# Performance work log

Measured on AMD Instinct MI355X. Metric: run time of the kernel, lower is better.

Reference implementation:

```python
import jax, jax.numpy as jnp
import numpy as np

N_M = 100000   # metric nodes
N_A = 20000    # alert nodes
E_C = 1600000  # metric->metric 'correlation' edges
E_K = 800000   # metric->alert 'cause' edges
F_IN = 64      # raw feature dim (lazy in_channels in PyG)
DIMS = [128, 256]  # out_dim // 2**(num_layers-i-1) for lstm_dim=256, num_layers=2
NEG_SLOPE = 0.01   # nn.LeakyReLU default


def _lin(key, fan_in, fan_out):
    s = 1.0 / np.sqrt(fan_in)
    return jax.random.uniform(key, (fan_in, fan_out), minval=-s, maxval=s, dtype=jnp.float32)


def setup_inputs() -> dict:
    key = jax.random.key(0)
    ks = jax.random.split(key, 32)
    inp = {
        'x_metric': jax.random.normal(ks[0], (N_M, F_IN), dtype=jnp.float32),
        'x_alert': jax.random.normal(ks[1], (N_A, F_IN), dtype=jnp.float32),
        'w_corr': jax.random.uniform(ks[2], (E_C,), dtype=jnp.float32),
        'w_cause': jax.random.uniform(ks[3], (E_K,), dtype=jnp.float32),
        'src_corr': jax.random.randint(ks[4], (E_C,), 0, N_M, dtype=jnp.int32),
        'dst_corr': jax.random.randint(ks[5], (E_C,), 0, N_M, dtype=jnp.int32),
        'src_cause': jax.random.randint(ks[6], (E_K,), 0, N_M, dtype=jnp.int32),
        'dst_cause': jax.random.randint(ks[7], (E_K,), 0, N_A, dtype=jnp.int32),
    }
    # GraphConv params: lin_rel (with bias) applied to aggregated messages,
    # lin_root (no bias) applied to destination features. Two convs per layer.
    kidx = 8
    in_m, in_a = F_IN, F_IN
    for li, d in enumerate(DIMS):
        inp[f'Wr_c{li}'] = _lin(ks[kidx], in_m, d); kidx += 1  # corr rel
        inp[f'br_c{li}'] = jnp.zeros((d,), jnp.float32)
        inp[f'Wo_c{li}'] = _lin(ks[kidx], in_m, d); kidx += 1  # corr root (dst=metric)
        inp[f'Wr_k{li}'] = _lin(ks[kidx], in_m, d); kidx += 1  # cause rel (src=metric)
        inp[f'br_k{li}'] = jnp.zeros((d,), jnp.float32)
        inp[f'Wo_k{li}'] = _lin(ks[kidx], in_a, d); kidx += 1  # cause root (dst=alert)
        in_m, in_a = d, d
    return inp


def _leaky(x):
    return jnp.where(x > 0, x, NEG_SLOPE * x)


def reference(x_metric, x_alert, w_corr, w_cause,
              src_corr, dst_corr, src_cause, dst_cause,
              Wr_c0, br_c0, Wo_c0, Wr_k0, br_k0, Wo_k0,
              Wr_c1, br_c1, Wo_c1, Wr_k1, br_k1, Wo_k1):
    xm, xa = x_metric, x_alert
    layers = [(Wr_c0, br_c0, Wo_c0, Wr_k0, br_k0, Wo_k0),
              (Wr_c1, br_c1, Wo_c1, Wr_k1, br_k1, Wo_k1)]
    for Wrc, brc, Woc, Wrk, brk, Wok in layers:
        # metric <- metric, GraphConv aggr='add'
        msg_c = xm[src_corr] * w_corr[:, None]                 # [E_C, d_in]
        agg_c = jax.ops.segment_sum(msg_c, dst_corr, num_segments=N_M)
        new_m = agg_c @ Wrc + brc + xm @ Woc
        # alert <- metric, GraphConv aggr='max' (empty segments -> 0, torch_scatter convention)
        msg_k = xm[src_cause] * w_cause[:, None]               # [E_K, d_in]
        agg_k = jax.ops.segment_max(msg_k, dst_cause, num_segments=N_A)
        agg_k = jnp.where(jnp.isfinite(agg_k), agg_k, 0.0)
        new_a = agg_k @ Wrk + brk + xa @ Wok
        xm = _leaky(new_m)
        xa = _leaky(new_a)
    return xa  # HGNN.forward returns x['alert']
```

## Files before the change

### kernel.cpp

```cpp
#include <hip/hip_runtime.h>

#define N_M 100000
#define N_A 20000
#define E_C 1600000
#define E_K 800000
#define CH 2048
#define NXCD 8

typedef __attribute__((ext_vector_type(8)))  short  short8_t;
typedef __attribute__((ext_vector_type(8)))  unsigned short ushort8_t;
typedef __attribute__((ext_vector_type(4)))  unsigned short ushort4_t;
typedef __attribute__((ext_vector_type(4)))  float  f32x4;

__device__ __forceinline__ unsigned short f2b(float f) {
    unsigned u = __float_as_uint(f);
    return (unsigned short)((u + 0x7fffu + ((u >> 16) & 1u)) >> 16);
}
__device__ __forceinline__ float b2f(unsigned short h) {
    return __uint_as_float((unsigned)h << 16);
}

__global__ __launch_bounds__(256) void cast_f32_bf16(const float* __restrict__ in,
                                                     unsigned short* __restrict__ out, int n) {
    int i = (blockIdx.x * 256 + threadIdx.x) * 4;
    if (i >= n) return;
    float4 v = *(const float4*)(in + i);
    ushort4_t o; o.x = f2b(v.x); o.y = f2b(v.y); o.z = f2b(v.z); o.w = f2b(v.w);
    *(ushort4_t*)(out + i) = o;
}

__global__ __launch_bounds__(256) void cast_weights(
    const float* rc0, const float* oc0, const float* rk0, const float* ok0,
    const float* rk1, const float* ok1, unsigned short* __restrict__ wb) {
    int i = (blockIdx.x * 256 + threadIdx.x) * 4;
    if (i >= 98304) return;
    const float* src; int off;
    if      (i < 8192)  { src = rc0; off = 0; }
    else if (i < 16384) { src = oc0; off = 8192; }
    else if (i < 24576) { src = rk0; off = 16384; }
    else if (i < 32768) { src = ok0; off = 24576; }
    else if (i < 65536) { src = rk1; off = 32768; }
    else                { src = ok1; off = 65536; }
    float4 v = *(const float4*)(src + (i - off));
    ushort4_t o; o.x = f2b(v.x); o.y = f2b(v.y); o.z = f2b(v.z); o.w = f2b(v.w);
    *(ushort4_t*)(wb + i) = o;
}


__global__ __launch_bounds__(256) void hist_part(const int* __restrict__ dst,
                                                 int* __restrict__ deg,
                                                 int nE, int nodes_per_part) {
    int chunk = blockIdx.x >> 3, part = blockIdx.x & 7;
    int lo = part * nodes_per_part, hi = lo + nodes_per_part;
    int base = chunk * CH + threadIdx.x;
    #pragma unroll
    for (int k = 0; k < 8; ++k) {
        int e = base + k * 256;
        if (e < nE) {
            int d = __builtin_nontemporal_load(dst + e);
            if (d >= lo && d < hi) atomicAdd(&deg[d], 1);
        }
    }
}

__global__ __launch_bounds__(256) void fill_pay_part(const int* __restrict__ dst,
                                                     const int* __restrict__ src,
                                                     const float* __restrict__ w,
                                                     int* __restrict__ cursor,
                                                     int2* __restrict__ csr_sw,
                                                     int nE, int nodes_per_part) {
    int chunk = blockIdx.x >> 3, part = blockIdx.x & 7;
    int lo = part * nodes_per_part, hi = lo + nodes_per_part;
    int base = chunk * CH + threadIdx.x;
    #pragma unroll
    for (int k = 0; k < 8; ++k) {
        int e = base + k * 256;
        if (e < nE) {
            int d = __builtin_nontemporal_load(dst + e);
            if (d >= lo && d < hi) {
                int p = atomicAdd(&cursor[d], 1);
                int2 sw;
                sw.x = __builtin_nontemporal_load(src + e);
                sw.y = __float_as_int(__builtin_nontemporal_load(w + e));
                csr_sw[p] = sw;
            }
        }
    }
}

__global__ __launch_bounds__(256) void scan_p1(const int* __restrict__ deg,
                                               int* __restrict__ partial, int n) {
    __shared__ int red[256];
    int base = blockIdx.x * CH + threadIdx.x;
    int s = 0;
    #pragma unroll
    for (int k = 0; k < 8; ++k) { int i = base + k * 256; if (i < n) s += deg[i]; }
    red[threadIdx.x] = s; __syncthreads();
    for (int off = 128; off > 0; off >>= 1) {
        if (threadIdx.x < off) red[threadIdx.x] += red[threadIdx.x + off];
        __syncthreads();
    }
    if (threadIdx.x == 0) partial[blockIdx.x] = red[0];
}

__global__ __launch_bounds__(64) void scan_p2(int* __restrict__ partial,
                                              int* __restrict__ rowptr_end, int P) {
    int lane = threadIdx.x;
    int v = (lane < P) ? partial[lane] : 0;
    int incl = v;
    for (int off = 1; off < 64; off <<= 1) {
        int t = __shfl_up(incl, off);
        if (lane >= off) incl += t;
    }
    if (lane < P) partial[lane] = incl - v;
    if (lane == 63) *rowptr_end = incl;
}

__global__ __launch_bounds__(256) void scan_p3(const int* __restrict__ deg,
                                               const int* __restrict__ partial,
                                               int* __restrict__ rowptr,
                                               int* __restrict__ cursor, int n) {
    __shared__ int buf[256];
    int base = blockIdx.x * CH;
    int v[8]; int lsum = 0;
    #pragma unroll
    for (int k = 0; k < 8; ++k) {
        int i = base + threadIdx.x * 8 + k;
        v[k] = (i < n) ? deg[i] : 0; lsum += v[k];
    }
    buf[threadIdx.x] = lsum; __syncthreads();
    for (int off = 1; off < 256; off <<= 1) {
        int t = (threadIdx.x >= off) ? buf[threadIdx.x - off] : 0;
        __syncthreads(); buf[threadIdx.x] += t; __syncthreads();
    }
    int excl = buf[threadIdx.x] - lsum + partial[blockIdx.x];
    #pragma unroll
    for (int k = 0; k < 8; ++k) {
        int i = base + threadIdx.x * 8 + k;
        if (i < n) { rowptr[i] = excl; cursor[i] = excl; }
        excl += v[k];
    }
}

__global__ __launch_bounds__(256) void agg_sum_d64_b(
    const unsigned short* __restrict__ x, const int2* __restrict__ csr_sw,
    const int* __restrict__ rowptr, unsigned short* __restrict__ out, int n) {
    int gw = blockIdx.x * 4 + (threadIdx.x >> 6);
    int lane = threadIdx.x & 63;
    if (gw >= n) return;
    int j = rowptr[gw], end = rowptr[gw + 1];
    float acc = 0.f;
    for (; j + 4 <= end; j += 4) {
        int2 e0 = csr_sw[j], e1 = csr_sw[j+1], e2 = csr_sw[j+2], e3 = csr_sw[j+3];
        float v0 = b2f(x[(size_t)e0.x * 64 + lane]);
        float v1 = b2f(x[(size_t)e1.x * 64 + lane]);
        float v2 = b2f(x[(size_t)e2.x * 64 + lane]);
        float v3 = b2f(x[(size_t)e3.x * 64 + lane]);
        acc = fmaf(v0, __int_as_float(e0.y), acc);
        acc = fmaf(v1, __int_as_float(e1.y), acc);
        acc = fmaf(v2, __int_as_float(e2.y), acc);
        acc = fmaf(v3, __int_as_float(e3.y), acc);
    }
    for (; j < end; ++j) {
        int2 e = csr_sw[j];
        acc = fmaf(b2f(x[(size_t)e.x * 64 + lane]), __int_as_float(e.y), acc);
    }
    out[(size_t)gw * 64 + lane] = f2b(acc);
}

__global__ __launch_bounds__(256) void agg_max_d64_b(
    const unsigned short* __restrict__ x, const int2* __restrict__ csr_sw,
    const int* __restrict__ rowptr, unsigned short* __restrict__ out, int n) {
    int gw = blockIdx.x * 4 + (threadIdx.x >> 6);
    int lane = threadIdx.x & 63;
    if (gw >= n) return;
    int beg = rowptr[gw], end = rowptr[gw + 1];
    float acc = -INFINITY;
    int j = beg;
    for (; j + 4 <= end; j += 4) {
        int2 e0 = csr_sw[j], e1 = csr_sw[j+1], e2 = csr_sw[j+2], e3 = csr_sw[j+3];
        acc = fmaxf(acc, b2f(x[(size_t)e0.x * 64 + lane]) * __int_as_float(e0.y));
        acc = fmaxf(acc, b2f(x[(size_t)e1.x * 64 + lane]) * __int_as_float(e1.y));
        acc = fmaxf(acc, b2f(x[(size_t)e2.x * 64 + lane]) * __int_as_float(e2.y));
        acc = fmaxf(acc, b2f(x[(size_t)e3.x * 64 + lane]) * __int_as_float(e3.y));
    }
    for (; j < end; ++j) {
        int2 e = csr_sw[j];
        acc = fmaxf(acc, b2f(x[(size_t)e.x * 64 + lane]) * __int_as_float(e.y));
    }
    if (beg == end) acc = 0.f;
    out[(size_t)gw * 64 + lane] = f2b(acc);
}

__global__ __launch_bounds__(256) void agg_max_d128_b(
    const unsigned short* __restrict__ x, const int2* __restrict__ csr_sw,
    const int* __restrict__ rowptr, unsigned short* __restrict__ out, int n) {
    int gw = blockIdx.x * 4 + (threadIdx.x >> 6);
    int lane = threadIdx.x & 63;
    if (gw >= n) return;
    int beg = rowptr[gw], end = rowptr[gw + 1];
    float ax = -INFINITY, ay = -INFINITY;
    int j = beg;
    for (; j + 2 <= end; j += 2) {
        int2 e0 = csr_sw[j], e1 = csr_sw[j+1];
        float w0 = __int_as_float(e0.y), w1 = __int_as_float(e1.y);
        unsigned v0 = ((const unsigned*)(x + (size_t)e0.x * 128))[lane];
        unsigned v1 = ((const unsigned*)(x + (size_t)e1.x * 128))[lane];
        ax = fmaxf(ax, b2f((unsigned short)(v0 & 0xffff)) * w0);
        ay = fmaxf(ay, b2f((unsigned short)(v0 >> 16)) * w0);
        ax = fmaxf(ax, b2f((unsigned short)(v1 & 0xffff)) * w1);
        ay = fmaxf(ay, b2f((unsigned short)(v1 >> 16)) * w1);
    }
    for (; j < end; ++j) {
        int2 e = csr_sw[j];
        float ww = __int_as_float(e.y);
        unsigned v = ((const unsigned*)(x + (size_t)e.x * 128))[lane];
        ax = fmaxf(ax, b2f((unsigned short)(v & 0xffff)) * ww);
        ay = fmaxf(ay, b2f((unsigned short)(v >> 16)) * ww);
    }
    if (beg == end) { ax = 0.f; ay = 0.f; }
    ((unsigned*)(out + (size_t)gw * 128))[lane] =
        (unsigned)f2b(ax) | ((unsigned)f2b(ay) << 16);
}

template <int K1, int K2, bool OBF>
__global__ __launch_bounds__(256) void dual_gemm_mfma(
    const unsigned short* __restrict__ A1, const unsigned short* __restrict__ A2,
    const unsigned short* __restrict__ B1, const unsigned short* __restrict__ B2,
    const float* __restrict__ bias, void* __restrict__ out, int M, int N) {
    constexpr int KTOT = K1 + K2;
    constexpr int LB = KTOT + 8;
    __shared__ __align__(16) unsigned short sA[128 * 40];
    __shared__ __align__(16) unsigned short sBT[64 * LB];

    const int tid = threadIdx.x;
    const int lane = tid & 63, wid = tid >> 6;
    const int wm = wid >> 1, wn = wid & 1;
    const int bm0 = blockIdx.y * 128, n0 = blockIdx.x * 64;

    for (int idx = tid; idx < KTOT * 64; idx += 256) {
        int k = idx >> 6, n = idx & 63;
        unsigned short v = (k < K1) ? B1[k * N + n0 + n] : B2[(k - K1) * N + n0 + n];
        sBT[n * LB + k] = v;
    }

    f32x4 acc[4][2];
    #pragma unroll
    for (int i = 0; i < 4; ++i)
        #pragma unroll
        for (int j = 0; j < 2; ++j)
            acc[i][j] = (f32x4){0.f, 0.f, 0.f, 0.f};

    const int kk = (lane >> 4) * 8;
    const int l15 = lane & 15;

    for (int k0 = 0; k0 < KTOT; k0 += 32) {
        __syncthreads();
        #pragma unroll
        for (int i = 0; i < 2; ++i) {
            int v = tid + i * 256;
            int row = v >> 2, kv = (v & 3) * 8;
            int gm = bm0 + row, gk = k0 + kv;
            ushort8_t val = (ushort8_t)0;
            if (gm < M) {
                const unsigned short* src = (gk < K1)
                    ? (A1 + (size_t)gm * K1 + gk)
                    : (A2 + (size_t)gm * K2 + (gk - K1));
                val = *(const ushort8_t*)src;
            }
            *(ushort8_t*)(sA + row * 40 + kv) = val;
        }
        __syncthreads();

        short8_t bfr[2];
        #pragma unroll
        for (int nf = 0; nf < 2; ++nf)
            bfr[nf] = *(const short8_t*)(sBT + (wn * 32 + nf * 16 + l15) * LB + k0 + kk);
        #pragma unroll
        for (int mf = 0; mf < 4; ++mf) {
            short8_t a = *(const short8_t*)(sA + (wm * 64 + mf * 16 + l15) * 40 + kk);
            acc[mf][0] = __builtin_amdgcn_mfma_f32_16x16x32_bf16(a, bfr[0], acc[mf][0], 0, 0, 0);
            acc[mf][1] = __builtin_amdgcn_mfma_f32_16x16x32_bf16(a, bfr[1], acc[mf][1], 0, 0, 0);
        }
    }

    #pragma unroll
    for (int nf = 0; nf < 2; ++nf) {
        int col = n0 + wn * 32 + nf * 16 + l15;
        float bcol = bias[col];
        #pragma unroll
        for (int mf = 0; mf < 4; ++mf) {
            int rowb = bm0 + wm * 64 + mf * 16 + (lane >> 4) * 4;
            #pragma unroll
            for (int i = 0; i < 4; ++i) {
                int r = rowb + i;
                if (r >= M) continue;
                float v = acc[mf][nf][i] + bcol;
                v = (v > 0.f) ? v : 0.01f * v;
                if (OBF) ((unsigned short*)out)[(size_t)r * N + col] = f2b(v);
                else     ((float*)out)[(size_t)r * N + col] = v;
            }
        }
    }
}

extern "C" void kernel_launch(void* const* d_in, const int* in_sizes, int n_in,
                              void* d_out, int out_size, void* d_ws, size_t ws_size,
                              hipStream_t stream) {
    const float* x_metric = (const float*)d_in[0];
    const float* x_alert  = (const float*)d_in[1];
    const float* w_corr   = (const float*)d_in[2];
    const float* w_cause  = (const float*)d_in[3];
    const int* src_corr   = (const int*)d_in[4];
    const int* dst_corr   = (const int*)d_in[5];
    const int* src_cause  = (const int*)d_in[6];
    const int* dst_cause  = (const int*)d_in[7];
    const float* Wr_c0 = (const float*)d_in[8];
    const float* br_c0 = (const float*)d_in[9];
    const float* Wo_c0 = (const float*)d_in[10];
    const float* Wr_k0 = (const float*)d_in[11];
    const float* br_k0 = (const float*)d_in[12];
    const float* Wo_k0 = (const float*)d_in[13];
    const float* Wr_k1 = (const float*)d_in[17];
    const float* br_k1 = (const float*)d_in[18];
    const float* Wo_k1 = (const float*)d_in[19];

    float* ws = (float*)d_ws;
    unsigned short* xh_m = (unsigned short*)(ws);
    unsigned short* xh_a = (unsigned short*)(ws + 3200000);
    unsigned short* wb   = (unsigned short*)(ws + 3840000);
    int*  corr_rowptr  = (int*)(ws + 3900000);
    int2* corr_sw      = (int2*)(ws + 4000064);
    int*  cause_rowptr = (int*)(ws + 7200064);
    int2* cause_sw     = (int2*)(ws + 7220128);
    int*  corr_cursor  = (int*)(ws + 8820128);
    int*  cause_cursor = (int*)(ws + 8920128);
    int*  corr_part    = (int*)(ws + 8940128);
    int*  cause_part   = (int*)(ws + 8940192);
    unsigned short* aggm  = (unsigned short*)(ws + 9000000);
    unsigned short* aggk0 = (unsigned short*)(ws + 12200000);
    unsigned short* xm0h  = (unsigned short*)(ws + 12840000);
    unsigned short* xa0h  = (unsigned short*)(ws + 19240000);
    unsigned short* aggk1 = (unsigned short*)(ws + 20520000);

    const unsigned short* Wb_rc0 = wb;
    const unsigned short* Wb_oc0 = wb + 8192;
    const unsigned short* Wb_rk0 = wb + 16384;
    const unsigned short* Wb_ok0 = wb + 24576;
    const unsigned short* Wb_rk1 = wb + 32768;
    const unsigned short* Wb_ok1 = wb + 65536;

    const int corr_chunks  = (E_C + CH - 1) / CH;
    const int cause_chunks = (E_K + CH - 1) / CH;
    const int corr_P  = (N_M + CH - 1) / CH;
    const int cause_P = (N_A + CH - 1) / CH;

    cast_f32_bf16<<<(N_M * 64 / 4 + 255) / 256, 256, 0, stream>>>(x_metric, xh_m, N_M * 64);
    cast_f32_bf16<<<(N_A * 64 / 4 + 255) / 256, 256, 0, stream>>>(x_alert, xh_a, N_A * 64);
    cast_weights<<<96, 256, 0, stream>>>(Wr_c0, Wo_c0, Wr_k0, Wo_k0, Wr_k1, Wo_k1, wb);

    hipMemsetAsync(corr_cursor, 0, (size_t)(N_M + N_A) * 4, stream);
    hist_part<<<corr_chunks * NXCD, 256, 0, stream>>>(dst_corr, corr_cursor, E_C, N_M / NXCD);
    hist_part<<<cause_chunks * NXCD, 256, 0, stream>>>(dst_cause, cause_cursor, E_K, N_A / NXCD);
    scan_p1<<<corr_P, 256, 0, stream>>>(corr_cursor, corr_part, N_M);
    scan_p1<<<cause_P, 256, 0, stream>>>(cause_cursor, cause_part, N_A);
    scan_p2<<<1, 64, 0, stream>>>(corr_part, corr_rowptr + N_M, corr_P);
    scan_p2<<<1, 64, 0, stream>>>(cause_part, cause_rowptr + N_A, cause_P);
    scan_p3<<<corr_P, 256, 0, stream>>>(corr_cursor, corr_part, corr_rowptr, corr_cursor, N_M);
    scan_p3<<<cause_P, 256, 0, stream>>>(cause_cursor, cause_part, cause_rowptr, cause_cursor, N_A);
    fill_pay_part<<<corr_chunks * NXCD, 256, 0, stream>>>(dst_corr, src_corr, w_corr,
                                                          corr_cursor, corr_sw, E_C, N_M / NXCD);
    fill_pay_part<<<cause_chunks * NXCD, 256, 0, stream>>>(dst_cause, src_cause, w_cause,
                                                           cause_cursor, cause_sw, E_K, N_A / NXCD);

    agg_sum_d64_b<<<(N_M + 3) / 4, 256, 0, stream>>>(xh_m, corr_sw, corr_rowptr, aggm, N_M);
    agg_max_d64_b<<<(N_A + 3) / 4, 256, 0, stream>>>(xh_m, cause_sw, cause_rowptr, aggk0, N_A);

    {   dim3 grid(128 / 64, (N_A + 127) / 128);
        dual_gemm_mfma<64, 64, true><<<grid, 256, 0, stream>>>(
            aggk0, xh_a, Wb_rk0, Wb_ok0, br_k0, xa0h, N_A, 128);
    }
    {   dim3 grid(128 / 64, (N_M + 127) / 128);
        dual_gemm_mfma<64, 64, true><<<grid, 256, 0, stream>>>(
            aggm, xh_m, Wb_rc0, Wb_oc0, br_c0, xm0h, N_M, 128);
    }

    agg_max_d128_b<<<(N_A + 3) / 4, 256, 0, stream>>>(xm0h, cause_sw, cause_rowptr, aggk1, N_A);
    {   dim3 grid(256 / 64, (N_A + 127) / 128);
        dual_gemm_mfma<128, 128, false><<<grid, 256, 0, stream>>>(
            aggk1, xa0h, Wb_rk1, Wb_ok1, br_k1, (float*)d_out, N_A, 256);
    }
}
```

Baseline: 589.9 us.

## Bucket edges by destination partition once before CSR histogram and fill

Before, the histogram and fill kernels each had eight blocks per edge chunk, one per destination partition, so every block reread the whole chunk and dropped edges outside its partition. Now a single pass reads dst, src and weight once and scatters each edge into one of eight per-partition buckets, using shared-memory counters and one global cursor per bucket. The histogram and fill kernels then read only their own bucket, and blockIdx&7 still keeps each partition's atomics on one XCD. The cost is an extra write and read of the bucketed edges, plus a fixed bucket capacity that silently drops edges if a partition overflows. That capacity leaves only a few percent of headroom over the uniform-random expectation.

```diff
diff --git a/kernel.cpp b/kernel.cpp
--- a/kernel.cpp
+++ b/kernel.cpp
@@ -5,7 +5,8 @@
 #define E_C 1600000
 #define E_K 800000
 #define CH 2048
-#define NXCD 8
+#define CAP_C 208192
+#define CAP_K 108192
 
 typedef __attribute__((ext_vector_type(8)))  short  short8_t;
 typedef __attribute__((ext_vector_type(8)))  unsigned short ushort8_t;
@@ -46,44 +47,70 @@
     *(ushort4_t*)(wb + i) = o;
 }
 
-
-__global__ __launch_bounds__(256) void hist_part(const int* __restrict__ dst,
-                                                 int* __restrict__ deg,
-                                                 int nE, int nodes_per_part) {
-    int chunk = blockIdx.x >> 3, part = blockIdx.x & 7;
-    int lo = part * nodes_per_part, hi = lo + nodes_per_part;
-    int base = chunk * CH + threadIdx.x;
-    #pragma unroll
-    for (int k = 0; k < 8; ++k) {
-        int e = base + k * 256;
+__global__ __launch_bounds__(256) void bucket_pass_t(
+    const int* __restrict__ dst, const int* __restrict__ src,
+    const float* __restrict__ w, int* __restrict__ bdst, int2* __restrict__ bsw,
+    int* __restrict__ gcur, int nE, int NPP, int CAP) {
+    __shared__ int cnt[8], base[8], off[8];
+    int t = threadIdx.x;
+    if (t < 8) { cnt[t] = 0; off[t] = 0; }
+    __syncthreads();
+    int e0 = blockIdx.x * CH + t;
+    int d[8], s[8], p[8]; float ww[8];
+    #pragma unroll
+    for (int k = 0; k < 8; ++k) {
+        int e = e0 + k * 256;
         if (e < nE) {
-            int d = __builtin_nontemporal_load(dst + e);
-            if (d >= lo && d < hi) atomicAdd(&deg[d], 1);
+            d[k]  = __builtin_nontemporal_load(dst + e);
+            s[k]  = __builtin_nontemporal_load(src + e);
+            ww[k] = __builtin_nontemporal_load(w + e);
+            p[k]  = d[k] / NPP;
+            atomicAdd(&cnt[p[k]], 1);
+        } else p[k] = -1;
+    }
+    __syncthreads();
+    if (t < 8) base[t] = atomicAdd(&gcur[t], cnt[t]);
+    __syncthreads();
+    #pragma unroll
+    for (int k = 0; k < 8; ++k) {
+        if (p[k] >= 0) {
+            int pos = base[p[k]] + atomicAdd(&off[p[k]], 1);
+            if (pos < CAP) {
+                bdst[p[k] * CAP + pos] = d[k];
+                bsw [p[k] * CAP + pos] = make_int2(s[k], __float_as_int(ww[k]));
+            }
         }
     }
 }
 
-__global__ __launch_bounds__(256) void fill_pay_part(const int* __restrict__ dst,
-                                                     const int* __restrict__ src,
-                                                     const float* __restrict__ w,
-                                                     int* __restrict__ cursor,
-                                                     int2* __restrict__ csr_sw,
-                                                     int nE, int nodes_per_part) {
-    int chunk = blockIdx.x >> 3, part = blockIdx.x & 7;
-    int lo = part * nodes_per_part, hi = lo + nodes_per_part;
-    int base = chunk * CH + threadIdx.x;
-    #pragma unroll
-    for (int k = 0; k < 8; ++k) {
-        int e = base + k * 256;
-        if (e < nE) {
-            int d = __builtin_nontemporal_load(dst + e);
-            if (d >= lo && d < hi) {
-                int p = atomicAdd(&cursor[d], 1);
-                int2 sw;
-                sw.x = __builtin_nontemporal_load(src + e);
-                sw.y = __float_as_int(__builtin_nontemporal_load(w + e));
-                csr_sw[p] = sw;
-            }
+__global__ __launch_bounds__(256) void hist_bkt(const int* __restrict__ bdst,
+                                                const int* __restrict__ gcur,
+                                                int* __restrict__ deg, int CAP) {
+    int part = blockIdx.x & 7, seg = blockIdx.x >> 3;
+    int n = min(gcur[part], CAP);
+    int i = seg * CH + threadIdx.x;
+    #pragma unroll
+    for (int k = 0; k < 8; ++k) {
+        int idx = i + k * 256;
+        if (idx < n) atomicAdd(&deg[bdst[part * CAP + idx]], 1);
+    }
+}
+
+__global__ __launch_bounds__(256) void fill_bkt(const int* __restrict__ bdst,
+                                                const int2* __restrict__ bsw,
+                                                const int* __restrict__ gcur,
+                                                int* __restrict__ cursor,
+                                                int2* __restrict__ csr_sw, int CAP) {
+    int part = blockIdx.x & 7, seg = blockIdx.x >> 3;
+    int n = min(gcur[part], CAP);
+    int i = seg * CH + threadIdx.x;
+    #pragma unroll
+    for (int k = 0; k < 8; ++k) {
+        int idx = i + k * 256;
+        if (idx < n) {
+            int d = bdst[part * CAP + idx];
+            int pos = atomicAdd(&cursor[d], 1);
+            csr_sw[pos] = bsw[part * CAP + idx];
         }
     }
 }
@@ -330,18 +357,24 @@
     unsigned short* xh_a = (unsigned short*)(ws + 3200000);
     unsigned short* wb   = (unsigned short*)(ws + 3840000);
     int*  corr_rowptr  = (int*)(ws + 3900000);
-    int2* corr_sw      = (int2*)(ws + 4000064);
-    int*  cause_rowptr = (int*)(ws + 7200064);
-    int2* cause_sw     = (int2*)(ws + 7220128);
-    int*  corr_cursor  = (int*)(ws + 8820128);
-    int*  cause_cursor = (int*)(ws + 8920128);
-    int*  corr_part    = (int*)(ws + 8940128);
-    int*  cause_part   = (int*)(ws + 8940192);
-    unsigned short* aggm  = (unsigned short*)(ws + 9000000);
-    unsigned short* aggk0 = (unsigned short*)(ws + 12200000);
-    unsigned short* xm0h  = (unsigned short*)(ws + 12840000);
-    unsigned short* xa0h  = (unsigned short*)(ws + 19240000);
-    unsigned short* aggk1 = (unsigned short*)(ws + 20520000);
+    int*  cause_rowptr = (int*)(ws + 4000016);
+    int*  corr_part    = (int*)(ws + 4020032);
+    int*  cause_part   = (int*)(ws + 4020096);
+    int*  corr_cursor  = (int*)(ws + 4020160);
+    int*  cause_cursor = (int*)(ws + 4120160);
+    int*  gcur_c       = (int*)(ws + 4140160);
+    int*  gcur_k       = (int*)(ws + 4140168);
+    int2* corr_sw      = (int2*)(ws + 4140176);
+    int2* cause_sw     = (int2*)(ws + 7340176);
+    int*  bkt_c_dst = (int*)(ws + 8940176);
+    int2* bkt_c_sw  = (int2*)(ws + 10605712);
+    int*  bkt_k_dst = (int*)(ws + 13936784);
+    int2* bkt_k_sw  = (int2*)(ws + 14802320);
+    unsigned short* aggm  = (unsigned short*)(ws + 8940176);
+    unsigned short* aggk0 = (unsigned short*)(ws + 12140176);
+    unsigned short* xm0h  = (unsigned short*)(ws + 12780176);
+    unsigned short* xa0h  = (unsigned short*)(ws + 19180176);
+    unsigned short* aggk1 = (unsigned short*)(ws + 20460176);
 
     const unsigned short* Wb_rc0 = wb;
     const unsigned short* Wb_oc0 = wb + 8192;
@@ -354,24 +387,32 @@
     const int cause_chunks = (E_K + CH - 1) / CH;
     const int corr_P  = (N_M + CH - 1) / CH;
     const int cause_P = (N_A + CH - 1) / CH;
+    const int corr_bsegs  = (CAP_C + CH - 1) / CH;
+    const int cause_bsegs = (CAP_K + CH - 1) / CH;
 
     cast_f32_bf16<<<(N_M * 64 / 4 + 255) / 256, 256, 0, stream>>>(x_metric, xh_m, N_M * 64);
     cast_f32_bf16<<<(N_A * 64 / 4 + 255) / 256, 256, 0, stream>>>(x_alert, xh_a, N_A * 64);
     cast_weights<<<96, 256, 0, stream>>>(Wr_c0, Wo_c0, Wr_k0, Wo_k0, Wr_k1, Wo_k1, wb);
 
-    hipMemsetAsync(corr_cursor, 0, (size_t)(N_M + N_A) * 4, stream);
-    hist_part<<<corr_chunks * NXCD, 256, 0, stream>>>(dst_corr, corr_cursor, E_C, N_M / NXCD);
-    hist_part<<<cause_chunks * NXCD, 256, 0, stream>>>(dst_cause, cause_cursor, E_K, N_A / NXCD);
+    hipMemsetAsync(corr_cursor, 0, (size_t)(N_M + N_A + 16) * 4, stream);
+    bucket_pass_t<<<corr_chunks, 256, 0, stream>>>(dst_corr, src_corr, w_corr,
+                                                   bkt_c_dst, bkt_c_sw, gcur_c,
+                                                   E_C, N_M / 8, CAP_C);
+    bucket_pass_t<<<cause_chunks, 256, 0, stream>>>(dst_cause, src_cause, w_cause,
+                                                    bkt_k_dst, bkt_k_sw, gcur_k,
+                                                    E_K, N_A / 8, CAP_K);
+    hist_bkt<<<corr_bsegs * 8, 256, 0, stream>>>(bkt_c_dst, gcur_c, corr_cursor, CAP_C);
+    hist_bkt<<<cause_bsegs * 8, 256, 0, stream>>>(bkt_k_dst, gcur_k, cause_cursor, CAP_K);
     scan_p1<<<corr_P, 256, 0, stream>>>(corr_cursor, corr_part, N_M);
     scan_p1<<<cause_P, 256, 0, stream>>>(cause_cursor, cause_part, N_A);
     scan_p2<<<1, 64, 0, stream>>>(corr_part, corr_rowptr + N_M, corr_P);
     scan_p2<<<1, 64, 0, stream>>>(cause_part, cause_rowptr + N_A, cause_P);
     scan_p3<<<corr_P, 256, 0, stream>>>(corr_cursor, corr_part, corr_rowptr, corr_cursor, N_M);
     scan_p3<<<cause_P, 256, 0, stream>>>(cause_cursor, cause_part, cause_rowptr, cause_cursor, N_A);
-    fill_pay_part<<<corr_chunks * NXCD, 256, 0, stream>>>(dst_corr, src_corr, w_corr,
-                                                          corr_cursor, corr_sw, E_C, N_M / NXCD);
-    fill_pay_part<<<cause_chunks * NXCD, 256, 0, stream>>>(dst_cause, src_cause, w_cause,
-                                                           cause_cursor, cause_sw, E_K, N_A / NXCD);
+    fill_bkt<<<corr_bsegs * 8, 256, 0, stream>>>(bkt_c_dst, bkt_c_sw, gcur_c,
+                                                 corr_cursor, corr_sw, CAP_C);
+    fill_bkt<<<cause_bsegs * 8, 256, 0, stream>>>(bkt_k_dst, bkt_k_sw, gcur_k,
+                                                  cause_cursor, cause_sw, CAP_K);
 
     agg_sum_d64_b<<<(N_M + 3) / 4, 256, 0, stream>>>(xh_m, corr_sw, corr_rowptr, aggm, N_M);
     agg_max_d64_b<<<(N_A + 3) / 4, 256, 0, stream>>>(xh_m, cause_sw, cause_rowptr, aggk0, N_A);
```

Measured after the change: 593.8 us. About the same (+0.7%).
